# Performance work log

Hardware: AMD Instinct MI355X
Metric: run time of the kernel (lower is better)

## Reference

```python
import jax, jax.numpy as jnp
import numpy as np

N_NODES = 50000
N_EDGES = 800000
IN_DIM = 8
EDGE_DIM = 4
HIDDEN = 16
OUT_DIM = 1


def _lin_init(key, fan_in, fan_out):
    kw, kb = jax.random.split(key)
    bound = 1.0 / np.sqrt(fan_in)
    W = jax.random.uniform(kw, (fan_in, fan_out), minval=-bound, maxval=bound, dtype=jnp.float32)
    b = jax.random.uniform(kb, (fan_out,), minval=-bound, maxval=bound, dtype=jnp.float32)
    return W, b


def setup_inputs() -> dict:
    key = jax.random.key(0)
    ks = jax.random.split(key, 16)
    x = jax.random.normal(ks[0], (N_NODES, IN_DIM), dtype=jnp.float32)
    edge_index = jax.random.randint(ks[1], (2, N_EDGES), 0, N_NODES, dtype=jnp.int32)
    edge_attr = jax.random.normal(ks[2], (N_EDGES, EDGE_DIM), dtype=jnp.float32)

    inp = {"x": x, "edge_index": edge_index, "edge_attr": edge_attr}
    in_dims = [IN_DIM, HIDDEN]
    for i in range(2):
        d_in = in_dims[i]
        W1, b1 = _lin_init(ks[3 + 4 * i], EDGE_DIM, HIDDEN)
        W2, b2 = _lin_init(ks[4 + 4 * i], HIDDEN, d_in * HIDDEN)
        root = jax.random.uniform(ks[5 + 4 * i], (d_in, HIDDEN), minval=-1.0 / np.sqrt(d_in), maxval=1.0 / np.sqrt(d_in), dtype=jnp.float32)
        bias = jnp.zeros((HIDDEN,), dtype=jnp.float32)
        inp[f"eW1_{i}"] = W1; inp[f"eb1_{i}"] = b1
        inp[f"eW2_{i}"] = W2; inp[f"eb2_{i}"] = b2
        inp[f"root_{i}"] = root; inp[f"bias_{i}"] = bias
    mW1, mb1 = _lin_init(ks[11], HIDDEN, HIDDEN)
    mW2, mb2 = _lin_init(ks[12], HIDDEN, OUT_DIM)
    inp["mW1"] = mW1; inp["mb1"] = mb1; inp["mW2"] = mW2; inp["mb2"] = mb2
    return inp


def _nnconv(x, src, dst, edge_attr, eW1, eb1, eW2, eb2, root, bias):
    # edge MLP -> per-edge weight matrix [E, d_in, HIDDEN]
    h = jax.nn.silu(edge_attr @ eW1 + eb1)
    Wedge = (h @ eW2 + eb2).reshape(edge_attr.shape[0], x.shape[1], HIDDEN)
    # gather source features, per-edge matmul, scatter-mean to targets
    msg = jnp.einsum('ei,eio->eo', x[src], Wedge)  # [E, HIDDEN]
    agg = jax.ops.segment_sum(msg, dst, num_segments=N_NODES)
    cnt = jax.ops.segment_sum(jnp.ones((msg.shape[0],), dtype=msg.dtype), dst, num_segments=N_NODES)
    agg = agg / jnp.maximum(cnt, 1.0)[:, None]
    return x @ root + agg + bias


def reference(x, edge_index, edge_attr,
              eW1_0, eb1_0, eW2_0, eb2_0, root_0, bias_0,
              eW1_1, eb1_1, eW2_1, eb2_1, root_1, bias_1,
              mW1, mb1, mW2, mb2):
    src, dst = edge_index[0], edge_index[1]
    x = jax.nn.relu(_nnconv(x, src, dst, edge_attr, eW1_0, eb1_0, eW2_0, eb2_0, root_0, bias_0))
    x = jax.nn.relu(_nnconv(x, src, dst, edge_attr, eW1_1, eb1_1, eW2_1, eb2_1, root_1, bias_1))
    out = jax.nn.sigmoid(jax.nn.silu(x @ mW1 + mb1) @ mW2 + mb2)
    return out
```

## Files before the change

kernel.cpp:

```cpp
#include <hip/hip_runtime.h>
#include <hip/hip_fp16.h>

#define NN 50000
#define NE 800000
#define NBUCK 392

__device__ __forceinline__ float sigm(float v) { return 1.0f / (1.0f + __expf(-v)); }


__global__ void sort_count(const int* __restrict__ ei,
                           int* __restrict__ cntA, int* __restrict__ cntB)
{
    __shared__ int hA[NBUCK], hB[NBUCK];
    int t = threadIdx.x;
    for (int i = t; i < NBUCK; i += 256) { hA[i] = 0; hB[i] = 0; }
    __syncthreads();
    int base = blockIdx.x * 2048;
#pragma unroll
    for (int r = 0; r < 8; ++r) {
        int idx = base + r * 256 + t;
        if (idx < NE) {
            int s = ei[idx], d = ei[NE + idx];
            atomicAdd(&hB[s >> 7], 1);
            atomicAdd(&hA[d >> 7], 1);
        }
    }
    __syncthreads();
    for (int i = t; i < NBUCK; i += 256) {
        if (hA[i]) atomicAdd(&cntA[i], hA[i]);
        if (hB[i]) atomicAdd(&cntB[i], hB[i]);
    }
}

__global__ void sort_scan(const int* __restrict__ cntA, const int* __restrict__ cntB,
                          int* __restrict__ baseA, int* __restrict__ baseB,
                          int* __restrict__ curA,  int* __restrict__ curB)
{
    __shared__ int a[512], b[512];
    int t = threadIdx.x;
    a[t] = (t < NBUCK) ? cntA[t] : 0;
    b[t] = (t < NBUCK) ? cntB[t] : 0;
    __syncthreads();
#pragma unroll
    for (int dd = 1; dd < 512; dd <<= 1) {
        int av = (t >= dd) ? a[t - dd] : 0;
        int bv = (t >= dd) ? b[t - dd] : 0;
        __syncthreads();
        a[t] += av; b[t] += bv;
        __syncthreads();
    }
    int exA = (t > 0) ? a[t - 1] : 0;
    int exB = (t > 0) ? b[t - 1] : 0;
    if (t < NBUCK) { baseA[t] = exA; curA[t] = exA; baseB[t] = exB; curB[t] = exB; }
    if (t == 511)  { baseA[NBUCK] = a[511]; baseB[NBUCK] = b[511]; }
}

__global__ __launch_bounds__(256) void sort_scatterA(const int* __restrict__ ei,
                                                     int* __restrict__ curA,
                                                     unsigned long long* __restrict__ recA)
{
    __shared__ int lcnt[NBUCK];
    __shared__ int lofs[NBUCK];
    int t = threadIdx.x;
    for (int i = t; i < NBUCK; i += 256) lcnt[i] = 0;
    __syncthreads();
    int base = blockIdx.x * 2048;
#pragma unroll
    for (int r = 0; r < 8; ++r) {
        int e = base + r * 256 + t;
        if (e < NE) atomicAdd(&lcnt[ei[NE + e] >> 7], 1);
    }
    __syncthreads();
    for (int i = t; i < NBUCK; i += 256)
        lofs[i] = lcnt[i] ? atomicAdd(&curA[i], lcnt[i]) : 0;
    __syncthreads();
#pragma unroll
    for (int r = 0; r < 8; ++r) {
        int e = base + r * 256 + t;
        if (e < NE) {
            int s = ei[e], d = ei[NE + e];
            int p = atomicAdd(&lofs[d >> 7], 1);
            recA[p] = ((unsigned long long)(unsigned)(d & 127) << 36)
                    | ((unsigned long long)(unsigned)s << 20)
                    | (unsigned long long)(unsigned)e;
        }
    }
}

__global__ __launch_bounds__(256) void sort_localAB(const unsigned long long* __restrict__ recA,
                                                    const int* __restrict__ baseA,
                                                    int* __restrict__ off_all,
                                                    int* __restrict__ curB,
                                                    unsigned long long* __restrict__ recB)
{
    __shared__ int c[128];
    __shared__ int live[128];
    __shared__ int lcnt[NBUCK];
    __shared__ int lofs[NBUCK];
    int t = threadIdx.x;
    int b = blockIdx.x;
    int lo = baseA[b], hi = baseA[b + 1];
    if (t < 128) c[t] = 0;
    for (int i = t; i < NBUCK; i += 256) lcnt[i] = 0;
    __syncthreads();
    for (int i = lo + t; i < hi; i += 256) {
        unsigned long long rec = recA[i];
        atomicAdd(&c[(int)(rec >> 36) & 127], 1);
        atomicAdd(&lcnt[(int)(rec >> 27) & 511], 1);
    }
    __syncthreads();
#pragma unroll
    for (int dd = 1; dd < 128; dd <<= 1) {
        int v = (t >= dd && t < 128) ? c[t - dd] : 0;
        __syncthreads();
        if (t < 128) c[t] += v;
        __syncthreads();
    }
    if (t < 128) {
        int ex = (t > 0) ? c[t - 1] : 0;
        int d = (b << 7) + t;
        if (d <= NN) off_all[d] = lo + ex;
        live[t] = lo + ex;
    }
    __syncthreads();
    for (int i = t; i < NBUCK; i += 256)
        lofs[i] = lcnt[i] ? atomicAdd(&curB[i], lcnt[i]) : 0;
    __syncthreads();
    for (int i = lo + t; i < hi; i += 256) {
        unsigned long long rec = recA[i];
        int dp = atomicAdd(&live[(int)(rec >> 36) & 127], 1);
        int s  = (int)((rec >> 20) & 0xFFFFu);
        int p  = atomicAdd(&lofs[s >> 7], 1);
        recB[p] = ((unsigned long long)(unsigned)(s & 127) << 40)
                | ((unsigned long long)(unsigned)dp << 20)
                | (rec & 0xFFFFFull);
    }
}

__global__ __launch_bounds__(256) void sort_localB(const unsigned long long* __restrict__ recB,
                                                   const int* __restrict__ baseB,
                                                   const float4* __restrict__ ea4,
                                                   int* __restrict__ off_all,
                                                   unsigned* __restrict__ sperm32,
                                                   float4* __restrict__ ea_perm)
{
    __shared__ int c[128];
    __shared__ int live[128];
    int t = threadIdx.x;
    int b = blockIdx.x;
    int lo = baseB[b], hi = baseB[b + 1];
    if (t < 128) c[t] = 0;
    __syncthreads();
    for (int i = lo + t; i < hi; i += 256)
        atomicAdd(&c[(int)(recB[i] >> 40) & 127], 1);
    __syncthreads();
#pragma unroll
    for (int dd = 1; dd < 128; dd <<= 1) {
        int v = (t >= dd && t < 128) ? c[t - dd] : 0;
        __syncthreads();
        if (t < 128) c[t] += v;
        __syncthreads();
    }
    if (t < 128) {
        int ex = (t > 0) ? c[t - 1] : 0;
        int s = (b << 7) + t;
        if (s <= NN) off_all[NN + s] = NE + lo + ex;
        live[t] = lo + ex;
    }
    __syncthreads();
    for (int i = lo + t; i < hi; i += 256) {
        unsigned long long rec = recB[i];
        int k = (int)(rec >> 40) & 127;
        int pos = atomicAdd(&live[k], 1);
        unsigned sl = (unsigned)(k & 15);
        unsigned dp = (unsigned)((rec >> 20) & 0xFFFFFu);
        sperm32[pos] = (sl << 20) | dp;
        ea_perm[pos] = ea4[rec & 0xFFFFFull];
    }
}

template<int DIN>
__global__ __launch_bounds__(256) void edge_fusedG(
        const float* __restrict__ xin,
        const unsigned* __restrict__ sperm32,
        const float4* __restrict__ ea_perm,
        const float* __restrict__ eW1,
        const float* __restrict__ eb1,
        const float* __restrict__ eW2,
        const float* __restrict__ eb2,
        const int*   __restrict__ off_all,
        __half* __restrict__ msgbuf)
{
    __shared__ __align__(16) float4 w2L4[4 * DIN * 17];
    __shared__ __align__(16) float4 G4[16 * 69];
    __shared__ __align__(16) float4 xbL[16 * 5];
    __shared__ __align__(16) float  xL[16 * DIN];
    __shared__ __align__(16) float  b2L[DIN * 16];
    __shared__ __align__(16) float4 w1t[16];
    __shared__ __align__(16) float  b1s[16];

    int tid = threadIdx.x;
    int nb  = blockIdx.x * 16;
    if (tid < 16) {
        w1t[tid] = make_float4(eW1[tid], eW1[16 + tid], eW1[32 + tid], eW1[48 + tid]);
        b1s[tid] = eb1[tid];
    }
    {
        float* w2f = (float*)w2L4;
        for (int t = tid; t < 16 * DIN * 16; t += 256) {
            int k = t / (DIN * 16);
            int rem = t - k * DIN * 16;
            int i = rem >> 4, o = rem & 15;
            w2f[((((o >> 2) * DIN + i) * 17) + k) * 4 + (o & 3)] = eW2[t];
        }
    }
    for (int t = tid; t < DIN * 16; t += 256) b2L[t] = eb2[t];
    for (int t = tid; t < 16 * DIN; t += 256) xL[t] = xin[(size_t)nb * DIN + t];
    __syncthreads();

    {
        int nl = tid >> 4, k = tid & 15;
        const float* xrow = xL + nl * DIN;
#pragma unroll
        for (int ob = 0; ob < 4; ++ob) {
            float4 a4 = make_float4(0.f, 0.f, 0.f, 0.f);
#pragma unroll
            for (int i = 0; i < DIN; ++i) {
                float4 w = w2L4[(ob * DIN + i) * 17 + k];
                a4.x += xrow[i] * w.x; a4.y += xrow[i] * w.y;
                a4.z += xrow[i] * w.z; a4.w += xrow[i] * w.w;
            }
            G4[nl * 69 + ob * 17 + k] = a4;
        }
        if (k < 4) {
            int ob = k;
            const float4* b2v = (const float4*)b2L;
            float4 a4 = make_float4(0.f, 0.f, 0.f, 0.f);
#pragma unroll
            for (int i = 0; i < DIN; ++i) {
                float4 b = b2v[i * 4 + ob];
                a4.x += xrow[i] * b.x; a4.y += xrow[i] * b.y;
                a4.z += xrow[i] * b.z; a4.w += xrow[i] * b.w;
            }
            xbL[nl * 5 + ob] = a4;
        }
    }
    __syncthreads();

    int eBeg = off_all[NN + nb] - NE;
    int eEnd = off_all[NN + nb + 16] - NE;
    for (int pos = eBeg + tid; pos < eEnd; pos += 256) {
        unsigned pk = sperm32[pos];
        int dp = (int)(pk & 0xFFFFFu);
        int sl = (int)(pk >> 20);
        float4 a = ea_perm[pos];

        float h[16];
#pragma unroll
        for (int j = 0; j < 16; ++j) {
            float4 w = w1t[j];
            float p = b1s[j] + a.x * w.x + a.y * w.y + a.z * w.z + a.w * w.w;
            h[j] = p * sigm(p);
        }
        float4 acc[4];
#pragma unroll
        for (int ob = 0; ob < 4; ++ob) acc[ob] = xbL[sl * 5 + ob];
#pragma unroll
        for (int k = 0; k < 16; ++k) {
            float hk = h[k];
#pragma unroll
            for (int ob = 0; ob < 4; ++ob) {
                float4 g = G4[sl * 69 + ob * 17 + k];
                acc[ob].x += hk * g.x; acc[ob].y += hk * g.y;
                acc[ob].z += hk * g.z; acc[ob].w += hk * g.w;
            }
        }
        __half2 h01 = __floats2half2_rn(acc[0].x, acc[0].y);
        __half2 h23 = __floats2half2_rn(acc[0].z, acc[0].w);
        __half2 h45 = __floats2half2_rn(acc[1].x, acc[1].y);
        __half2 h67 = __floats2half2_rn(acc[1].z, acc[1].w);
        __half2 h89 = __floats2half2_rn(acc[2].x, acc[2].y);
        __half2 hAB = __floats2half2_rn(acc[2].z, acc[2].w);
        __half2 hCD = __floats2half2_rn(acc[3].x, acc[3].y);
        __half2 hEF = __floats2half2_rn(acc[3].z, acc[3].w);
        uint4 w0 = make_uint4(*(unsigned*)&h01, *(unsigned*)&h23,
                              *(unsigned*)&h45, *(unsigned*)&h67);
        uint4 w1 = make_uint4(*(unsigned*)&h89, *(unsigned*)&hAB,
                              *(unsigned*)&hCD, *(unsigned*)&hEF);
        uint4* dst = (uint4*)(msgbuf + (size_t)dp * 16);
        dst[0] = w0;
        dst[1] = w1;
    }
}

__device__ __forceinline__ float gather_msg16(const __half* __restrict__ msgbuf,
                                              int s0, int e0, int tid)
{
    int half = (tid >> 3) & 1;
    int p    = tid & 7;
    float ax = 0.f, ay = 0.f;
    for (int j = s0 + half; j < e0; j += 2) {
        __half2 hv = *((const __half2*)(msgbuf + (size_t)j * 16) + p);
        float2 f = __half22float2(hv);
        ax += f.x; ay += f.y;
    }
    ax += __shfl_xor(ax, 8, 16);
    ay += __shfl_xor(ay, 8, 16);
    int ch = tid & 15;
    float vx = __shfl(ax, ch >> 1, 16);
    float vy = __shfl(ay, ch >> 1, 16);
    return (ch & 1) ? vy : vx;
}

__global__ __launch_bounds__(256) void gather_L0(
        const float* __restrict__ xin,
        const float* __restrict__ root,
        const float* __restrict__ bias,
        const int*   __restrict__ off_all,
        const __half* __restrict__ msgbuf,
        float* __restrict__ x1)
{
    __shared__ __align__(16) float rootL[8 * 16];
    __shared__ __align__(16) float biasL[16];
    int tid = threadIdx.x;
    if (tid < 128) rootL[tid] = root[tid];
    if (tid < 16) biasL[tid] = bias[tid];
    __syncthreads();

    int ch = tid & 15;
    int n  = blockIdx.x * 16 + (tid >> 4);
    int s0 = off_all[n], e0 = off_all[n + 1];

    float acc = gather_msg16(msgbuf, s0, e0, tid);
    float v = acc / fmaxf((float)(e0 - s0), 1.0f) + biasL[ch];
#pragma unroll
    for (int i = 0; i < 8; ++i)
        v += xin[(size_t)n * 8 + i] * rootL[i * 16 + ch];
    x1[(size_t)n * 16 + ch] = fmaxf(v, 0.f);
}

__global__ __launch_bounds__(256) void gather_final(
        const float* __restrict__ x1,
        const float* __restrict__ root,
        const float* __restrict__ bias,
        const int*   __restrict__ off_all,
        const __half* __restrict__ msgbuf,
        const float* __restrict__ mW1,
        const float* __restrict__ mb1,
        const float* __restrict__ mW2,
        const float* __restrict__ mb2,
        float* __restrict__ out)
{
    __shared__ __align__(16) float rootL[256];
    __shared__ __align__(16) float biasL[16];
    __shared__ __align__(16) float w1m[256];
    __shared__ __align__(16) float b1m[16];
    __shared__ __align__(16) float w2m[16];
    __shared__ float b2m;
    int tid = threadIdx.x;
    rootL[tid] = root[tid];
    w1m[tid] = mW1[tid];
    if (tid < 16) { biasL[tid] = bias[tid]; b1m[tid] = mb1[tid]; w2m[tid] = mW2[tid]; }
    if (tid == 0) b2m = mb2[0];
    __syncthreads();

    int ch = tid & 15;
    int n  = blockIdx.x * 16 + (tid >> 4);
    int s0 = off_all[n], e0 = off_all[n + 1];

    float acc = gather_msg16(msgbuf, s0, e0, tid);
    float v = acc / fmaxf((float)(e0 - s0), 1.0f) + biasL[ch];
#pragma unroll
    for (int i = 0; i < 16; ++i)
        v += x1[(size_t)n * 16 + i] * rootL[i * 16 + ch];
    v = fmaxf(v, 0.f);

    float z = b1m[ch];
#pragma unroll
    for (int o = 0; o < 16; ++o) {
        float vo = __shfl(v, o, 16);
        z += vo * w1m[o * 16 + ch];
    }
    float ss = z * sigm(z) * w2m[ch];
#pragma unroll
    for (int off = 8; off; off >>= 1) ss += __shfl_xor(ss, off, 16);
    if (ch == 0) out[n] = sigm(ss + b2m);
}

extern "C" void kernel_launch(void* const* d_in, const int* in_sizes, int n_in,
                              void* d_out, int out_size, void* d_ws, size_t ws_size,
                              hipStream_t stream) {
    const float* x     = (const float*)d_in[0];
    const int*   ei    = (const int*)  d_in[1];
    const float* ea    = (const float*)d_in[2];
    const float* eW1_0 = (const float*)d_in[3];
    const float* eb1_0 = (const float*)d_in[4];
    const float* eW2_0 = (const float*)d_in[5];
    const float* eb2_0 = (const float*)d_in[6];
    const float* root0 = (const float*)d_in[7];
    const float* bias0 = (const float*)d_in[8];
    const float* eW1_1 = (const float*)d_in[9];
    const float* eb1_1 = (const float*)d_in[10];
    const float* eW2_1 = (const float*)d_in[11];
    const float* eb2_1 = (const float*)d_in[12];
    const float* root1 = (const float*)d_in[13];
    const float* bias1 = (const float*)d_in[14];
    const float* mW1   = (const float*)d_in[15];
    const float* mb1   = (const float*)d_in[16];
    const float* mW2   = (const float*)d_in[17];
    const float* mb2   = (const float*)d_in[18];
    float* out = (float*)d_out;

    const int GG  = NN / 16;
    const int SBK = (NE + 2047) / 2048;

    int* W = (int*)d_ws;
    int* off_all = W;
    int* cntA    = W + 100004;
    int* cntB    = W + 100400;
    int* baseA   = W + 100800;
    int* baseB   = W + 101200;
    int* curA    = W + 101600;
    int* curB    = W + 102000;
    unsigned* sperm32 = (unsigned*)(W + 102400);
    float4* ea_perm   = (float4*)(W + 902400);
    float*  x1        = (float*)(W + 4102400);
    __half* msgbuf    = (__half*)(W + 4902400);
    unsigned long long* recA = (unsigned long long*)(W + 4902400);
    unsigned long long* recB = (unsigned long long*)(W + 6502400);

    hipMemsetAsync(cntA, 0, 2 * 396 * sizeof(int), stream);
    sort_count   <<<SBK,  256, 0, stream>>>(ei, cntA, cntB);
    sort_scan    <<<1,    512, 0, stream>>>(cntA, cntB, baseA, baseB, curA, curB);
    sort_scatterA<<<SBK,  256, 0, stream>>>(ei, curA, recA);
    sort_localAB <<<NBUCK,256, 0, stream>>>(recA, baseA, off_all, curB, recB);
    sort_localB  <<<NBUCK,256, 0, stream>>>(recB, baseB, (const float4*)ea,
                                            off_all, sperm32, ea_perm);

    edge_fusedG<8><<<GG, 256, 0, stream>>>(x, sperm32, ea_perm, eW1_0, eb1_0,
                                           eW2_0, eb2_0, off_all, msgbuf);
    gather_L0<<<GG, 256, 0, stream>>>(x, root0, bias0, off_all, msgbuf, x1);

    edge_fusedG<16><<<GG, 256, 0, stream>>>(x1, sperm32, ea_perm, eW1_1, eb1_1,
                                            eW2_1, eb2_1, off_all, msgbuf);
    gather_final<<<GG, 256, 0, stream>>>(x1, root1, bias1, off_all, msgbuf,
                                         mW1, mb1, mW2, mb2, out);
}
```

Measured before the change: 275.7 us.

## Halve edge-kernel W2 shared staging and double edges per sort block

The edge kernel now stages the second edge-MLP weight matrix into shared memory in two halves of the input dimension, accumulating into registers. This shrinks the shared-memory footprint (significant for DIN=16), which may allow more resident blocks per CU, at the cost of extra barriers and a second staging pass. Separately, the sort count and scatter kernels each process 4096 edges per block instead of 2048, halving the block count and the number of global atomics on bucket counters.

Measured after the change: 282.5 us. 2.5% more time.

```diff
diff --git a/kernel.cpp b/kernel.cpp
--- a/kernel.cpp
+++ b/kernel.cpp
@@ -15,9 +15,9 @@
     int t = threadIdx.x;
     for (int i = t; i < NBUCK; i += 256) { hA[i] = 0; hB[i] = 0; }
     __syncthreads();
-    int base = blockIdx.x * 2048;
-#pragma unroll
-    for (int r = 0; r < 8; ++r) {
+    int base = blockIdx.x * 4096;
+#pragma unroll
+    for (int r = 0; r < 16; ++r) {
         int idx = base + r * 256 + t;
         if (idx < NE) {
             int s = ei[idx], d = ei[NE + idx];
@@ -64,9 +64,9 @@
     int t = threadIdx.x;
     for (int i = t; i < NBUCK; i += 256) lcnt[i] = 0;
     __syncthreads();
-    int base = blockIdx.x * 2048;
-#pragma unroll
-    for (int r = 0; r < 8; ++r) {
+    int base = blockIdx.x * 4096;
+#pragma unroll
+    for (int r = 0; r < 16; ++r) {
         int e = base + r * 256 + t;
         if (e < NE) atomicAdd(&lcnt[ei[NE + e] >> 7], 1);
     }
@@ -75,7 +75,7 @@
         lofs[i] = lcnt[i] ? atomicAdd(&curA[i], lcnt[i]) : 0;
     __syncthreads();
 #pragma unroll
-    for (int r = 0; r < 8; ++r) {
+    for (int r = 0; r < 16; ++r) {
         int e = base + r * 256 + t;
         if (e < NE) {
             int s = ei[e], d = ei[NE + e];
@@ -191,7 +191,8 @@
         const int*   __restrict__ off_all,
         __half* __restrict__ msgbuf)
 {
-    __shared__ __align__(16) float4 w2L4[4 * DIN * 17];
+    constexpr int H = DIN / 2;
+    __shared__ __align__(16) float4 w2h[4 * H * 17];
     __shared__ __align__(16) float4 G4[16 * 69];
     __shared__ __align__(16) float4 xbL[16 * 5];
     __shared__ __align__(16) float  xL[16 * DIN];
@@ -205,44 +206,55 @@
         w1t[tid] = make_float4(eW1[tid], eW1[16 + tid], eW1[32 + tid], eW1[48 + tid]);
         b1s[tid] = eb1[tid];
     }
-    {
-        float* w2f = (float*)w2L4;
-        for (int t = tid; t < 16 * DIN * 16; t += 256) {
-            int k = t / (DIN * 16);
-            int rem = t - k * DIN * 16;
-            int i = rem >> 4, o = rem & 15;
-            w2f[((((o >> 2) * DIN + i) * 17) + k) * 4 + (o & 3)] = eW2[t];
-        }
-    }
     for (int t = tid; t < DIN * 16; t += 256) b2L[t] = eb2[t];
     for (int t = tid; t < 16 * DIN; t += 256) xL[t] = xin[(size_t)nb * DIN + t];
-    __syncthreads();
 
     {
         int nl = tid >> 4, k = tid & 15;
-        const float* xrow = xL + nl * DIN;
-#pragma unroll
-        for (int ob = 0; ob < 4; ++ob) {
-            float4 a4 = make_float4(0.f, 0.f, 0.f, 0.f);
-#pragma unroll
-            for (int i = 0; i < DIN; ++i) {
-                float4 w = w2L4[(ob * DIN + i) * 17 + k];
-                a4.x += xrow[i] * w.x; a4.y += xrow[i] * w.y;
-                a4.z += xrow[i] * w.z; a4.w += xrow[i] * w.w;
+        float4 a4[4];
+#pragma unroll
+        for (int ob = 0; ob < 4; ++ob) a4[ob] = make_float4(0.f, 0.f, 0.f, 0.f);
+
+#pragma unroll
+        for (int step = 0; step < 2; ++step) {
+            __syncthreads();
+            {
+                float* w2f = (float*)w2h;
+                for (int t = tid; t < 16 * H * 16; t += 256) {
+                    int kk = t / (H * 16);
+                    int rem = t - kk * (H * 16);
+                    int i = rem >> 4, o = rem & 15;
+                    w2f[((((o >> 2) * H + i) * 17) + kk) * 4 + (o & 3)] =
+                        eW2[kk * (DIN * 16) + (step * H + i) * 16 + o];
+                }
             }
-            G4[nl * 69 + ob * 17 + k] = a4;
-        }
+            __syncthreads();
+            const float* xrow = xL + nl * DIN + step * H;
+#pragma unroll
+            for (int ob = 0; ob < 4; ++ob) {
+#pragma unroll
+                for (int i = 0; i < H; ++i) {
+                    float4 w = w2h[(ob * H + i) * 17 + k];
+                    a4[ob].x += xrow[i] * w.x; a4[ob].y += xrow[i] * w.y;
+                    a4[ob].z += xrow[i] * w.z; a4[ob].w += xrow[i] * w.w;
+                }
+            }
+        }
+#pragma unroll
+        for (int ob = 0; ob < 4; ++ob) G4[nl * 69 + ob * 17 + k] = a4[ob];
+
         if (k < 4) {
             int ob = k;
             const float4* b2v = (const float4*)b2L;
-            float4 a4 = make_float4(0.f, 0.f, 0.f, 0.f);
+            const float* xrow = xL + nl * DIN;
+            float4 a = make_float4(0.f, 0.f, 0.f, 0.f);
 #pragma unroll
             for (int i = 0; i < DIN; ++i) {
-                float4 b = b2v[i * 4 + ob];
-                a4.x += xrow[i] * b.x; a4.y += xrow[i] * b.y;
-                a4.z += xrow[i] * b.z; a4.w += xrow[i] * b.w;
+                float4 bb = b2v[i * 4 + ob];
+                a.x += xrow[i] * bb.x; a.y += xrow[i] * bb.y;
+                a.z += xrow[i] * bb.z; a.w += xrow[i] * bb.w;
             }
-            xbL[nl * 5 + ob] = a4;
+            xbL[nl * 5 + ob] = a;
         }
     }
     __syncthreads();
@@ -412,7 +424,7 @@
     float* out = (float*)d_out;
 
     const int GG  = NN / 16;
-    const int SBK = (NE + 2047) / 2048;
+    const int SBK = (NE + 4095) / 4096;
 
     int* W = (int*)d_ws;
     int* off_all = W;
```
